# Kernel tuning notes

Measured on AMD Instinct MI355X. Metric: run time of the kernel, lower is better.

Reference implementation:

```python
import jax, jax.numpy as jnp
import numpy as np

B, N, D, F_IN, F_OUT, MAX_DEG = 256, 512, 6, 128, 128, 6


def setup_inputs() -> dict:
    key = jax.random.key(0)
    k_atoms, k_deg, k_idx, k_w, k_b = jax.random.split(key, 5)
    atoms = jax.random.normal(k_atoms, (B, N, F_IN), dtype=jnp.float32)
    # structured edges: per-atom degree in [0, MAX_DEG-1], valid neighbor ids in
    # the first `deg` slots, -1 padding afterwards (NGFP convention)
    deg = jax.random.randint(k_deg, (B, N, 1), 0, MAX_DEG)
    nbr = jax.random.randint(k_idx, (B, N, D), 0, N)
    slot = jnp.arange(D)[None, None, :]
    edges = jnp.where(slot < deg, nbr, -1).astype(jnp.int64)
    W = jax.random.normal(k_w, (MAX_DEG, F_IN, F_OUT), dtype=jnp.float32) * (1.0 / np.sqrt(F_IN))
    b = jax.random.normal(k_b, (MAX_DEG, F_OUT), dtype=jnp.float32) * 0.01
    return {"atoms": atoms, "edges": edges, "W": W, "b": b}


def reference(atoms, edges, W, b):
    # lookup_neighbors with include_self=True: gather neighbor rows (-1 -> zero row)
    atoms_p = jnp.pad(atoms, ((0, 0), (1, 0), (0, 0)))          # [B, N+1, F]; row 0 is zeros
    gathered = jax.vmap(lambda a, e: a[e])(atoms_p, edges + 1)  # [B, N, D, F]
    summed = gathered.sum(axis=-2) + atoms                      # [B, N, F] (self included)
    degrees = (edges != -1).sum(axis=-1, keepdims=True)         # [B, N, 1]
    out = jnp.zeros(summed.shape[:-1] + (W.shape[-1],), dtype=summed.dtype)
    for d in range(MAX_DEG):
        h = jax.nn.relu(summed @ W[d] + b[d])                   # [B, N, F_OUT]
        out = out + h * (degrees == d).astype(summed.dtype)
    return out
```

## Files before the change

kernel.cpp:

```cpp
#include <hip/hip_runtime.h>


typedef short bf16x8 __attribute__((ext_vector_type(8)));
typedef float f32x4  __attribute__((ext_vector_type(4)));
typedef unsigned short ushort_t;
typedef unsigned int uint_t;

constexpr int Nn = 512;
constexpr int Ff = 128;
constexpr int BN = 256 * 512;
constexpr int ROWSTRIDE = 34;

constexpr size_t WS_GC     = 0;
constexpr size_t WS_REGION = 256;
constexpr size_t WS_WT     = 256 + (size_t)6 * BN * 4;
constexpr size_t WS_SUMMED = WS_WT + 196608;
constexpr size_t WS_NEEDED = WS_SUMMED + (size_t)BN * 128 * 2;

__device__ inline ushort_t f2bf(float f) {
    uint_t u = __float_as_uint(f);
    return (ushort_t)((u + 0x7FFFu + ((u >> 16) & 1u)) >> 16);
}

__device__ inline bool detect_is64(const int* edges32) {
    int probe = edges32[2 * (threadIdx.x & 63) + 1];
    return __any(probe > 0) == 0;
}

__global__ __launch_bounds__(256, 2)
void k1_pre(const float* __restrict__ atoms,
            const int*   __restrict__ edges32,
            const float* __restrict__ W,
            int* __restrict__ gcnt,
            int* __restrict__ region,
            ushort_t* __restrict__ Wt,
            ushort_t* __restrict__ summed) {
    const int tid   = threadIdx.x;
    const int mol   = blockIdx.x >> 2;
    const int slice = blockIdx.x & 3;
    const bool is64 = detect_is64(edges32);

    __shared__ float    Arows[Nn * ROWSTRIDE];
    __shared__ ushort_t nbp[Nn * 6];
    __shared__ int      hist[6], base_sh[6];

    if (blockIdx.x < 384) {
        int linear = blockIdx.x * 256 + tid;
        int d = linear >> 14, rem = linear & 16383;
        int k = rem >> 7, n = rem & 127;
        Wt[d * 16384 + n * 128 + k] = f2bf(W[linear]);
    }

    {
        const size_t ebase = (size_t)mol * (Nn * 6);
        for (int i = tid; i < Nn * 6; i += 256) {
            int e = is64 ? edges32[(ebase + i) * 2] : edges32[ebase + i];
            nbp[i] = (ushort_t)(e >= 0 ? e : 0xFFFF);
        }
    }

    {
        const float4* gsrc = (const float4*)(atoms + (size_t)mol * (Nn * Ff) + slice * 32);
        #pragma unroll
        for (int it = 0; it < 16; it++) {
            int idx = tid + it * 256;
            int row = idx >> 3, q = idx & 7;
            float4 v = gsrc[row * 32 + q];
            int la = row * ROWSTRIDE + q * 4;
            float2 p0; p0.x = v.x; p0.y = v.y;
            float2 p1; p1.x = v.z; p1.y = v.w;
            *(float2*)&Arows[la]     = p0;
            *(float2*)&Arows[la + 2] = p1;
        }
    }
    __syncthreads();

    if (slice == 0) {
        if (tid < 6) hist[tid] = 0;
        __syncthreads();
        int dg[2], rk[2];
        #pragma unroll
        for (int s = 0; s < 2; s++) {
            int row = tid + s * 256;
            int dd = 0;
            #pragma unroll
            for (int j = 0; j < 6; j++) dd += (nbp[row * 6 + j] != 0xFFFF) ? 1 : 0;
            dg[s] = dd;
            rk[s] = atomicAdd(&hist[dd], 1);
        }
        __syncthreads();
        if (tid < 6) base_sh[tid] = atomicAdd(&gcnt[tid], hist[tid]);
        __syncthreads();
        #pragma unroll
        for (int s = 0; s < 2; s++)
            region[dg[s] * BN + base_sh[dg[s]] + rk[s]] = mol * Nn + tid + s * 256;
    }

    const int h = tid & 3, cbase = h * 8;
    #pragma unroll
    for (int rd = 0; rd < 8; rd++) {
        const int row = rd * 64 + (tid >> 2);
        float2 acc[4];
        #pragma unroll
        for (int c = 0; c < 4; c++)
            acc[c] = *(const float2*)&Arows[row * ROWSTRIDE + cbase + 2 * c];
        #pragma unroll
        for (int j = 0; j < 6; j++) {
            int e = nbp[row * 6 + j];
            if (e != 0xFFFF) {
                const float* src = &Arows[e * ROWSTRIDE + cbase];
                #pragma unroll
                for (int c = 0; c < 4; c++) {
                    float2 v = *(const float2*)&src[2 * c];
                    acc[c].x += v.x; acc[c].y += v.y;
                }
            }
        }
        uint4 o;
        o.x = (uint_t)f2bf(acc[0].x) | ((uint_t)f2bf(acc[0].y) << 16);
        o.y = (uint_t)f2bf(acc[1].x) | ((uint_t)f2bf(acc[1].y) << 16);
        o.z = (uint_t)f2bf(acc[2].x) | ((uint_t)f2bf(acc[2].y) << 16);
        o.w = (uint_t)f2bf(acc[3].x) | ((uint_t)f2bf(acc[3].y) << 16);
        *(uint4*)(summed + (size_t)(mol * Nn + row) * Ff + slice * 32 + cbase) = o;
    }
}

__global__ __launch_bounds__(256, 4)
void k2_gemm(const ushort_t* __restrict__ summed,
             const float*    __restrict__ bias,
             const ushort_t* __restrict__ Wt,
             const int*      __restrict__ region,
             const int*      __restrict__ gcnt,
             float*          __restrict__ out) {
    int cnts[6];
    #pragma unroll
    for (int dd = 0; dd < 6; dd++) cnts[dd] = gcnt[dd];
    const int bid = blockIdx.x;
    int d = -1, t = 0, accum = 0;
    #pragma unroll
    for (int dd = 0; dd < 6; dd++) {
        int tl = (cnts[dd] + 127) >> 7;
        if (d < 0 && bid < accum + tl) { d = dd; t = bid - accum; }
        accum += tl;
    }
    if (d < 0) return;
    const int count = cnts[d];
    const int m0 = t * 128;
    const int nrows = min(128, count - m0);

    __shared__ __attribute__((aligned(16))) ushort_t Bsh[128 * 136];
    __shared__ int ids[128];

    const int tid = threadIdx.x;
    if (tid < 128) {
        int idx = m0 + tid;
        if (idx >= count) idx = count - 1;
        ids[tid] = region[d * BN + idx];
    }
    {
        const uint4* Wg = (const uint4*)(Wt + (size_t)d * 16384);
        #pragma unroll
        for (int i = 0; i < 8; i++) {
            int idx = tid + i * 256;
            int n = idx >> 4, c = idx & 15;
            *(uint4*)&Bsh[n * 136 + c * 8] = Wg[idx];
        }
    }
    __syncthreads();

    const int lane = tid & 63, w = tid >> 6;
    const int mrow = w * 32;
    const int kq = lane >> 4;
    const int ml = lane & 15;

    bf16x8 af[2][4];
    #pragma unroll
    for (int mt = 0; mt < 2; mt++) {
        const int row = ids[mrow + mt * 16 + ml];
        const bf16x8* sp = (const bf16x8*)(summed + (size_t)row * Ff + kq * 8);
        #pragma unroll
        for (int k0 = 0; k0 < 4; k0++) af[mt][k0] = sp[k0 * 4];
    }

    #pragma unroll
    for (int nt = 0; nt < 8; nt++) {
        bf16x8 bfr[4];
        #pragma unroll
        for (int k0 = 0; k0 < 4; k0++)
            bfr[k0] = *(const bf16x8*)&Bsh[(nt * 16 + ml) * 136 + k0 * 32 + kq * 8];
        f32x4 c0 = {0.f, 0.f, 0.f, 0.f}, c1 = {0.f, 0.f, 0.f, 0.f};
        #pragma unroll
        for (int k0 = 0; k0 < 4; k0++) {
            c0 = __builtin_amdgcn_mfma_f32_16x16x32_bf16(af[0][k0], bfr[k0], c0, 0, 0, 0);
            c1 = __builtin_amdgcn_mfma_f32_16x16x32_bf16(af[1][k0], bfr[k0], c1, 0, 0, 0);
        }
        const int col = nt * 16 + ml;
        const float bcol = bias[d * Ff + col];
        #pragma unroll
        for (int mt = 0; mt < 2; mt++) {
            f32x4 cc = mt ? c1 : c0;
            #pragma unroll
            for (int reg = 0; reg < 4; reg++) {
                int rl = mrow + mt * 16 + kq * 4 + reg;
                if (rl < nrows) {
                    float v = cc[reg] + bcol;
                    out[(size_t)ids[rl] * Ff + col] = v > 0.f ? v : 0.f;
                }
            }
        }
    }
}

__global__ __launch_bounds__(128, 2)
void graphconv_fallback(const float* __restrict__ atoms,
                        const int* __restrict__ edges_raw,
                        const float* __restrict__ W,
                        const float* __restrict__ bias,
                        float* __restrict__ out) {
    const int tid = threadIdx.x;
    const int d = blockIdx.x % 6;
    const int k = blockIdx.x / 6;
    const int a0 = k * 256;
    __shared__ int eds[256 * 6];
    __shared__ int list[256];
    __shared__ int cnt;
    __shared__ float sv[2][Ff];
    bool is64;
    { int v = edges_raw[2 * (tid & 63) + 1]; is64 = (__ballot(v > 0) == 0ull); }
    if (!is64) { for (int i = tid; i < 256 * 6; i += 128) eds[i] = edges_raw[a0 * 6 + i]; }
    else       { for (int i = tid; i < 256 * 6; i += 128) eds[i] = edges_raw[2 * (a0 * 6 + i)]; }
    if (tid == 0) cnt = 0;
    __syncthreads();
    for (int i = tid; i < 256; i += 128) {
        int deg = 0;
        #pragma unroll
        for (int j = 0; j < 6; j++) deg += (eds[i * 6 + j] != -1) ? 1 : 0;
        if (deg == d) { int p = atomicAdd(&cnt, 1); list[p] = i; }
    }
    float Wreg[Ff];
    { const float* Wd = W + (size_t)d * Ff * Ff;
      #pragma unroll
      for (int f = 0; f < Ff; f++) Wreg[f] = Wd[f * Ff + tid]; }
    const float breg = bias[d * Ff + tid];
    __syncthreads();
    const int n = cnt;
    const float* batch_atoms = atoms + (size_t)(a0 / Nn) * Nn * Ff;
    const int row0 = a0 % Nn;
    for (int ii = 0; ii < n; ii++) {
        const int i = list[ii];
        float s = batch_atoms[(row0 + i) * Ff + tid];
        #pragma unroll
        for (int j = 0; j < 6; j++) {
            int e = eds[i * 6 + j];
            if (e != -1) s += batch_atoms[e * Ff + tid];
        }
        float* buf = sv[ii & 1];
        buf[tid] = s;
        __syncthreads();
        float acc = breg;
        const float4* sv4 = (const float4*)buf;
        #pragma unroll
        for (int fc = 0; fc < Ff / 4; fc++) {
            float4 x = sv4[fc];
            acc = fmaf(x.x, Wreg[4 * fc + 0], acc);
            acc = fmaf(x.y, Wreg[4 * fc + 1], acc);
            acc = fmaf(x.z, Wreg[4 * fc + 2], acc);
            acc = fmaf(x.w, Wreg[4 * fc + 3], acc);
        }
        out[(size_t)(a0 + i) * Ff + tid] = fmaxf(acc, 0.0f);
    }
}

extern "C" void kernel_launch(void* const* d_in, const int* in_sizes, int n_in,
                              void* d_out, int out_size, void* d_ws, size_t ws_size,
                              hipStream_t stream) {
    const float* atoms = (const float*)d_in[0];
    const int*   edges = (const int*)d_in[1];
    const float* W     = (const float*)d_in[2];
    const float* bias  = (const float*)d_in[3];
    float*       outp  = (float*)d_out;

    if (ws_size >= WS_NEEDED) {
        char* ws = (char*)d_ws;
        int*      gcnt   = (int*)(ws + WS_GC);
        int*      region = (int*)(ws + WS_REGION);
        ushort_t* Wt     = (ushort_t*)(ws + WS_WT);
        ushort_t* summed = (ushort_t*)(ws + WS_SUMMED);

        hipMemsetAsync(gcnt, 0, 32, stream);
        k1_pre<<<1024, 256, 0, stream>>>(atoms, edges, W, gcnt, region, Wt, summed);
        k2_gemm<<<1030, 256, 0, stream>>>(summed, bias, Wt, region, gcnt, outp);
    } else {
        graphconv_fallback<<<3072, 128, 0, stream>>>(atoms, edges, W, bias, outp);
    }
}
```

Baseline: 165.8 us.

## Split gather into 16-wide feature slices with XOR-swizzled float4 LDS layout

The preprocessing kernel now splits each molecule's 128 features into 8 slices of 16 instead of 4 slices of 32. That halves the shared-memory tile and lets the kernel raise launch bounds to 4 blocks per CU over twice as many blocks. The padded stride-34 float layout is replaced by an XOR-swizzled float4 layout, so the neighbor gather reads two float4s per row per thread instead of four float2s, with fewer bank conflicts. Neighbor indices are also read as packed 32-bit words. In exchange, each molecule's edge list is loaded and converted by eight blocks instead of four, and atoms rows are fetched in 64-byte chunks.

```diff
diff --git a/kernel.cpp b/kernel.cpp
--- a/kernel.cpp
+++ b/kernel.cpp
@@ -9,7 +9,6 @@
 constexpr int Nn = 512;
 constexpr int Ff = 128;
 constexpr int BN = 256 * 512;
-constexpr int ROWSTRIDE = 34;
 
 constexpr size_t WS_GC     = 0;
 constexpr size_t WS_REGION = 256;
@@ -27,7 +26,7 @@
     return __any(probe > 0) == 0;
 }
 
-__global__ __launch_bounds__(256, 2)
+__global__ __launch_bounds__(256, 4)
 void k1_pre(const float* __restrict__ atoms,
             const int*   __restrict__ edges32,
             const float* __restrict__ W,
@@ -36,11 +35,11 @@
             ushort_t* __restrict__ Wt,
             ushort_t* __restrict__ summed) {
     const int tid   = threadIdx.x;
-    const int mol   = blockIdx.x >> 2;
-    const int slice = blockIdx.x & 3;
+    const int mol   = blockIdx.x >> 3;
+    const int slice = blockIdx.x & 7;
     const bool is64 = detect_is64(edges32);
 
-    __shared__ float    Arows[Nn * ROWSTRIDE];
+    __shared__ float4   A4[Nn * 4];
     __shared__ ushort_t nbp[Nn * 6];
     __shared__ int      hist[6], base_sh[6];
 
@@ -60,17 +59,13 @@
     }
 
     {
-        const float4* gsrc = (const float4*)(atoms + (size_t)mol * (Nn * Ff) + slice * 32);
-        #pragma unroll
-        for (int it = 0; it < 16; it++) {
+        const float4* gsrc = (const float4*)(atoms + (size_t)mol * (Nn * Ff) + slice * 16);
+        #pragma unroll
+        for (int it = 0; it < 8; it++) {
             int idx = tid + it * 256;
-            int row = idx >> 3, q = idx & 7;
+            int row = idx >> 2, q = idx & 3;
             float4 v = gsrc[row * 32 + q];
-            int la = row * ROWSTRIDE + q * 4;
-            float2 p0; p0.x = v.x; p0.y = v.y;
-            float2 p1; p1.x = v.z; p1.y = v.w;
-            *(float2*)&Arows[la]     = p0;
-            *(float2*)&Arows[la + 2] = p1;
+            A4[row * 4 + (q ^ (row & 3))] = v;
         }
     }
     __syncthreads();
@@ -96,32 +91,34 @@
             region[dg[s] * BN + base_sh[dg[s]] + rk[s]] = mol * Nn + tid + s * 256;
     }
 
-    const int h = tid & 3, cbase = h * 8;
-    #pragma unroll
-    for (int rd = 0; rd < 8; rd++) {
-        const int row = rd * 64 + (tid >> 2);
-        float2 acc[4];
-        #pragma unroll
-        for (int c = 0; c < 4; c++)
-            acc[c] = *(const float2*)&Arows[row * ROWSTRIDE + cbase + 2 * c];
+    const int h = tid & 1, qb = 2 * (tid & 1);
+    const uint_t* np = (const uint_t*)nbp;
+    #pragma unroll
+    for (int rd = 0; rd < 4; rd++) {
+        const int row = rd * 128 + (tid >> 1);
+        uint_t u0 = np[row * 3], u1 = np[row * 3 + 1], u2 = np[row * 3 + 2];
+        int e[6] = { (int)(u0 & 0xFFFFu), (int)(u0 >> 16),
+                     (int)(u1 & 0xFFFFu), (int)(u1 >> 16),
+                     (int)(u2 & 0xFFFFu), (int)(u2 >> 16) };
+        int sb = row * 4 + (qb ^ (row & 3));
+        float4 a0 = A4[sb];
+        float4 a1 = A4[sb ^ 1];
         #pragma unroll
         for (int j = 0; j < 6; j++) {
-            int e = nbp[row * 6 + j];
-            if (e != 0xFFFF) {
-                const float* src = &Arows[e * ROWSTRIDE + cbase];
-                #pragma unroll
-                for (int c = 0; c < 4; c++) {
-                    float2 v = *(const float2*)&src[2 * c];
-                    acc[c].x += v.x; acc[c].y += v.y;
-                }
+            if (e[j] != 0xFFFF) {
+                int nb = e[j] * 4 + (qb ^ (e[j] & 3));
+                float4 v0 = A4[nb];
+                float4 v1 = A4[nb ^ 1];
+                a0.x += v0.x; a0.y += v0.y; a0.z += v0.z; a0.w += v0.w;
+                a1.x += v1.x; a1.y += v1.y; a1.z += v1.z; a1.w += v1.w;
             }
         }
         uint4 o;
-        o.x = (uint_t)f2bf(acc[0].x) | ((uint_t)f2bf(acc[0].y) << 16);
-        o.y = (uint_t)f2bf(acc[1].x) | ((uint_t)f2bf(acc[1].y) << 16);
-        o.z = (uint_t)f2bf(acc[2].x) | ((uint_t)f2bf(acc[2].y) << 16);
-        o.w = (uint_t)f2bf(acc[3].x) | ((uint_t)f2bf(acc[3].y) << 16);
-        *(uint4*)(summed + (size_t)(mol * Nn + row) * Ff + slice * 32 + cbase) = o;
+        o.x = (uint_t)f2bf(a0.x) | ((uint_t)f2bf(a0.y) << 16);
+        o.y = (uint_t)f2bf(a0.z) | ((uint_t)f2bf(a0.w) << 16);
+        o.z = (uint_t)f2bf(a1.x) | ((uint_t)f2bf(a1.y) << 16);
+        o.w = (uint_t)f2bf(a1.z) | ((uint_t)f2bf(a1.w) << 16);
+        *(uint4*)(summed + (size_t)(mol * Nn + row) * Ff + slice * 16 + h * 8) = o;
     }
 }
 
@@ -288,7 +285,7 @@
         ushort_t* summed = (ushort_t*)(ws + WS_SUMMED);
 
         hipMemsetAsync(gcnt, 0, 32, stream);
-        k1_pre<<<1024, 256, 0, stream>>>(atoms, edges, W, gcnt, region, Wt, summed);
+        k1_pre<<<2048, 256, 0, stream>>>(atoms, edges, W, gcnt, region, Wt, summed);
         k2_gemm<<<1030, 256, 0, stream>>>(summed, bias, Wt, region, gcnt, outp);
     } else {
         graphconv_fallback<<<3072, 128, 0, stream>>>(atoms, edges, W, bias, outp);
```

Measured after the change: 171.4 us. +3.4%, slower.
